# Optimization experiments

Hardware: AMD Instinct MI355X
Metric: run time of the kernel (lower is better)

## Reference

```python
import jax, jax.numpy as jnp
import numpy as np

EMB_DIM = 1024
ATT_DIM = 1024

def setup_inputs() -> dict:
    key = jax.random.key(0)
    ks = jax.random.split(key, 7)
    B, S = 8, 2048
    x_h = jax.random.normal(ks[0], (B, S, EMB_DIM), dtype=jnp.float32)
    # Linear params (stored as [in, out] for x @ W + b)
    sq = 1.0 / np.sqrt(EMB_DIM)
    Wq = jax.random.uniform(ks[1], (EMB_DIM, ATT_DIM), jnp.float32, -sq, sq)
    bq = jax.random.uniform(ks[2], (ATT_DIM,), jnp.float32, -sq, sq)
    Wk = jax.random.uniform(ks[3], (EMB_DIM, ATT_DIM), jnp.float32, -sq, sq)
    bk = jax.random.uniform(ks[4], (ATT_DIM,), jnp.float32, -sq, sq)
    Wv = jax.random.uniform(ks[5], (EMB_DIM, EMB_DIM), jnp.float32, -sq, sq)
    bv = jax.random.uniform(ks[6], (EMB_DIM,), jnp.float32, -sq, sq)
    return {"x_h": x_h, "Wq": Wq, "bq": bq, "Wk": Wk, "bk": bk, "Wv": Wv, "bv": bv}

def reference(x_h, Wq, bq, Wk, bk, Wv, bv):
    q = x_h @ Wq + bq               # [B,S,att_dim]
    k = x_h @ Wk + bk               # [B,S,att_dim]
    v = x_h @ Wv + bv               # [B,S,emb_dim]
    scale = 1.0 / jnp.sqrt(jnp.asarray(k.shape[-1], q.dtype))
    scores = jnp.einsum('bqd,bkd->bqk', q, k) * scale   # [B,S,S]
    # NOTE: original softmaxes over dim=1 (the QUERY axis), not the key axis.
    attn = jax.nn.softmax(scores, axis=1)
    return jnp.einsum('bqk,bkd->bqd', attn, v)
```

## Files before the change

kernel.cpp:

```cpp
#include <hip/hip_runtime.h>
#include <math.h>

typedef __bf16 bf16x8 __attribute__((ext_vector_type(8)));
typedef float f32x4 __attribute__((ext_vector_type(4)));
typedef unsigned short ushort8 __attribute__((ext_vector_type(8)));
typedef unsigned short ushort4v __attribute__((ext_vector_type(4)));
typedef unsigned short u16;

#define DEVINL __device__ __forceinline__

DEVINL u16 f2bf(float f) {
    union { float f; unsigned u; } a; a.f = f;
    unsigned u = a.u;
    return (u16)((u + 0x7FFFu + ((u >> 16) & 1u)) >> 16);
}
DEVINL float bf2f(u16 h) { return __uint_as_float(((unsigned)h) << 16); }

DEVINL void gload_lds16(const void* g, void* l) {
    __builtin_amdgcn_global_load_lds(
        (__attribute__((address_space(1))) void*)(g),
        (__attribute__((address_space(3))) void*)(l),
        16, 0, 0);
}

template<int EPI>
__global__ __launch_bounds__(512, 2)
void gemm256(const u16* __restrict__ A, int lda, long sAz,
             const u16* __restrict__ B, int ldb, long sBz,
             void* __restrict__ Cv, int ldc, long sCz,
             const float* __restrict__ bias, float* __restrict__ part,
             float scale, int K)
{
    __shared__ u16 lds[65536];
    const int tid = threadIdx.x;
    const int tile_x = blockIdx.x, tile_y = blockIdx.y;
    const long bz = blockIdx.z;

    const u16* Ab = A + bz * sAz;
    const u16* Bb = B + bz * sBz;
    const int row0 = tile_x * 256, col0 = tile_y * 256;

    const int sr = tid >> 2;
    const int csw = ((tid & 3) * 16) ^ (((sr >> 1) & 3) << 4);
    const u16* Ag = Ab + (long)(row0 + sr) * lda + (csw >> 1);
    const u16* Bg = Bb + (long)(col0 + sr) * ldb + (csw >> 1);
    const int dst0 = tid * 8;

    const int lane = tid & 63, wid = tid >> 6;
    const int wm = wid >> 2, wn = wid & 3;
    const int lane_r = lane & 15;
    const int rdcol = (((lane >> 4) * 16) ^ (((lane_r >> 1) & 3) << 4)) >> 1;
    const int arow0 = wm * 128 + lane_r;
    const int brow0 = wn * 64 + lane_r;

    const int NP = K >> 5;
    f32x4 acc[8][4] = {};

    auto issuePair = [&](int j2) {
        const int r = (j2 & 3) * 8192;
        const u16* ga = Ag + (long)j2 * 32;
        const u16* gb = Bg + (long)j2 * 32;
        gload_lds16(ga,                      &lds[r + dst0]);
        gload_lds16(ga + (long)128 * lda,    &lds[r + 4096 + dst0]);
        gload_lds16(gb,                      &lds[32768 + r + dst0]);
        gload_lds16(gb + (long)128 * ldb,    &lds[32768 + r + 4096 + dst0]);
    };

#define PHASE_BODY(JV)                                                      \
    {                                                                       \
        const int r = ((JV) & 3) * 8192;                                    \
        bf16x8 bfr[4], af[8];                                               \
        _Pragma("unroll")                                                   \
        for (int n = 0; n < 4; ++n)                                         \
            bfr[n] = *(const bf16x8*)&lds[32768 + r +                       \
                         (brow0 + n * 16) * 32 + rdcol];                    \
        _Pragma("unroll")                                                   \
        for (int m = 0; m < 8; ++m)                                         \
            af[m] = *(const bf16x8*)&lds[r + (arow0 + m * 16) * 32 + rdcol];\
        __builtin_amdgcn_s_setprio(1);                                      \
        _Pragma("unroll")                                                   \
        for (int m = 0; m < 8; ++m)                                         \
            _Pragma("unroll")                                               \
            for (int n = 0; n < 4; ++n)                                     \
                acc[m][n] = __builtin_amdgcn_mfma_f32_16x16x32_bf16(        \
                    bfr[n], af[m], acc[m][n], 0, 0, 0);                     \
        __builtin_amdgcn_s_setprio(0);                                      \
    }

    issuePair(0); issuePair(1); issuePair(2);
    asm volatile("s_waitcnt vmcnt(8)" ::: "memory");
    __builtin_amdgcn_s_barrier();

    for (int j = 0; j < NP - 3; ++j) {
        issuePair(j + 3);
        PHASE_BODY(j);
        asm volatile("s_waitcnt vmcnt(8)" ::: "memory");
        __builtin_amdgcn_s_barrier();
    }
    PHASE_BODY(NP - 3);
    asm volatile("s_waitcnt vmcnt(4)" ::: "memory");
    __builtin_amdgcn_s_barrier();
    PHASE_BODY(NP - 2);
    asm volatile("s_waitcnt vmcnt(0)" ::: "memory");
    __builtin_amdgcn_s_barrier();
    PHASE_BODY(NP - 1);
#undef PHASE_BODY

    const int erow = lane & 15, ecol0 = (lane >> 4) * 4;
    float4 bias4[4];
    if constexpr (EPI == 0) {
#pragma unroll
        for (int nf = 0; nf < 4; ++nf)
            bias4[nf] = *(const float4*)&bias[col0 + wn * 64 + nf * 16 + ecol0];
    }
    f32x4 csum[4] = {};
#pragma unroll
    for (int mf = 0; mf < 8; ++mf) {
        const int gr = row0 + wm * 128 + mf * 16 + erow;
#pragma unroll
        for (int nf = 0; nf < 4; ++nf) {
            const int gc = col0 + wn * 64 + nf * 16 + ecol0;
            f32x4 v = acc[mf][nf];
            if constexpr (EPI == 0) {
                v[0] += bias4[nf].x; v[1] += bias4[nf].y;
                v[2] += bias4[nf].z; v[3] += bias4[nf].w;
                ushort4v o = { f2bf(v[0]), f2bf(v[1]), f2bf(v[2]), f2bf(v[3]) };
                *(ushort4v*)((u16*)Cv + bz * sCz + (long)gr * ldc + gc) = o;
            } else if constexpr (EPI == 1) {
                f32x4 e;
#pragma unroll
                for (int r = 0; r < 4; ++r) e[r] = __expf(v[r] * scale);
                csum[nf] += e;
                ushort4v o = { f2bf(e[0]), f2bf(e[1]), f2bf(e[2]), f2bf(e[3]) };
                *(ushort4v*)((u16*)Cv + bz * sCz + (long)gr * ldc + gc) = o;
            } else {
                *(float4*)((float*)Cv + bz * sCz + (long)gr * ldc + gc) =
                    make_float4(v[0], v[1], v[2], v[3]);
            }
        }
    }
    if constexpr (EPI == 1) {
#pragma unroll
        for (int nf = 0; nf < 4; ++nf)
#pragma unroll
            for (int r = 0; r < 4; ++r) {
                float s = csum[nf][r];
                s += __shfl_xor(s, 1);
                s += __shfl_xor(s, 2);
                s += __shfl_xor(s, 4);
                s += __shfl_xor(s, 8);
                csum[nf][r] = s;
            }
        if ((lane & 15) == 0) {
#pragma unroll
            for (int nf = 0; nf < 4; ++nf) {
                float* p = part + ((bz * 16 + (long)tile_x * 2 + wm) * 2048)
                         + col0 + wn * 64 + nf * 16 + ecol0;
                *(float4*)p = make_float4(csum[nf][0], csum[nf][1],
                                          csum[nf][2], csum[nf][3]);
            }
        }
    }
}

__global__ void cast_x_k(const float* __restrict__ x, u16* __restrict__ o)
{
    const int i = blockIdx.x * 256 + threadIdx.x;
    const float4* xv = (const float4*)x;
    const float4 a = xv[(long)i * 2], b = xv[(long)i * 2 + 1];
    ushort8 r;
    r[0] = f2bf(a.x); r[1] = f2bf(a.y); r[2] = f2bf(a.z); r[3] = f2bf(a.w);
    r[4] = f2bf(b.x); r[5] = f2bf(b.y); r[6] = f2bf(b.z); r[7] = f2bf(b.w);
    *(ushort8*)(o + (long)i * 8) = r;
}

__global__ void wt_k(const float* __restrict__ Wq, const float* __restrict__ Wk,
                     const float* __restrict__ Wv, u16* __restrict__ Wt)
{
    __shared__ float t[32][33];
    const int z = blockIdx.z;
    const float* W = (z == 0) ? Wq : ((z == 1) ? Wk : Wv);
    const int k0 = blockIdx.x * 32, n0 = blockIdx.y * 32;
    const int tx = threadIdx.x, ty = threadIdx.y;
#pragma unroll
    for (int j = 0; j < 32; j += 8)
        t[ty + j][tx] = W[(long)(k0 + ty + j) * 1024 + n0 + tx];
    __syncthreads();
#pragma unroll
    for (int j = 0; j < 32; j += 8)
        Wt[((long)z * 1024 + n0 + ty + j) * 1024 + k0 + tx] = f2bf(t[tx][ty + j]);
}

__global__ void bias_k(const float* __restrict__ bq, const float* __restrict__ bk,
                       const float* __restrict__ bv, float* __restrict__ bcat)
{
    const int i = blockIdx.x * 256 + threadIdx.x;
    bcat[i] = (i < 1024) ? bq[i] : ((i < 2048) ? bk[i - 1024] : bv[i - 2048]);
}

__global__ void rcp_k(const float* __restrict__ part, float* __restrict__ rden)
{
    const int b = blockIdx.y;
    const int k = blockIdx.x * 256 + threadIdx.x;
    float s = 0.f;
#pragma unroll
    for (int c = 0; c < 16; ++c) s += part[((long)b * 16 + c) * 2048 + k];
    rden[b * 2048 + k] = 1.0f / s;
}

__global__ void vt_k(const u16* __restrict__ qkv, const float* __restrict__ rden,
                     u16* __restrict__ Vt)
{
    __shared__ float t[32][33];
    const int b = blockIdx.z;
    const int k0 = blockIdx.x * 32, d0 = blockIdx.y * 32;
    const int tx = threadIdx.x, ty = threadIdx.y;
#pragma unroll
    for (int j = 0; j < 32; j += 8) {
        const int k = k0 + ty + j;
        t[ty + j][tx] = bf2f(qkv[((long)b * 2048 + k) * 3072 + 2048 + d0 + tx])
                        * rden[b * 2048 + k];
    }
    __syncthreads();
#pragma unroll
    for (int j = 0; j < 32; j += 8)
        Vt[((long)b * 1024 + d0 + ty + j) * 2048 + k0 + tx] = f2bf(t[tx][ty + j]);
}

extern "C" void kernel_launch(void* const* d_in, const int* in_sizes, int n_in,
                              void* d_out, int out_size, void* d_ws, size_t ws_size,
                              hipStream_t stream)
{
    const float* x  = (const float*)d_in[0];
    const float* Wq = (const float*)d_in[1];
    const float* bq = (const float*)d_in[2];
    const float* Wk = (const float*)d_in[3];
    const float* bk = (const float*)d_in[4];
    const float* Wv = (const float*)d_in[5];
    const float* bv = (const float*)d_in[6];

    char* ws = (char*)d_ws;
    u16*   qkv  = (u16*)(ws);
    u16*   E    = (u16*)(ws + 100663296);
    u16*   Vt   = (u16*)(ws + 167772160);
    u16*   xb   = (u16*)(ws + 201326592);
    u16*   Wt   = (u16*)(ws + 234881024);
    float* bcat = (float*)(ws + 241172480);
    float* part = (float*)(ws + 241184768);
    float* rden = (float*)(ws + 243281920);

    const long sQKV = (long)2048 * 3072;
    const long sE   = (long)2048 * 2048;
    const long sVt  = (long)1024 * 2048;
    const long sO   = (long)2048 * 1024;

    cast_x_k<<<8192, 256, 0, stream>>>(x, xb);
    wt_k<<<dim3(32, 32, 3), dim3(32, 8), 0, stream>>>(Wq, Wk, Wv, Wt);
    bias_k<<<12, 256, 0, stream>>>(bq, bk, bv, bcat);
    gemm256<0><<<dim3(64, 12, 1), 512, 0, stream>>>(
        xb, 1024, 0, Wt, 1024, 0, qkv, 3072, 0, bcat, nullptr, 0.f, 1024);
    gemm256<1><<<dim3(8, 8, 8), 512, 0, stream>>>(
        qkv, 3072, sQKV, qkv + 1024, 3072, sQKV, E, 2048, sE,
        nullptr, part, 0.03125f, 1024);
    rcp_k<<<dim3(8, 8), 256, 0, stream>>>(part, rden);
    vt_k<<<dim3(64, 32, 8), dim3(32, 8), 0, stream>>>(qkv, rden, Vt);
    gemm256<2><<<dim3(8, 4, 8), 512, 0, stream>>>(
        E, 2048, sE, Vt, 2048, sVt, d_out, 1024, sO,
        nullptr, nullptr, 1.f, 2048);
}
```

Measured before the change: 307.8 us.

## Shrink GEMM tiles to 256x128 with double-buffered LDS and higher occupancy

Replaces the 256x256 tile with a 4-stage LDS ring by a 256x128 tile with a 2-stage double buffer. Each of the 8 waves now computes a 64x64 sub-tile, and launch bounds allow 4 blocks per CU. Grids double, and the softmax partial-sum layout and its reduction grow from 16 to 32 chunks. The aim is more blocks for better CU fill and latency hiding, at the cost of lower arithmetic intensity per tile, a shallower prefetch pipeline, and a full vmcnt(0) wait every K step.

```diff
diff --git a/kernel.cpp b/kernel.cpp
--- a/kernel.cpp
+++ b/kernel.cpp
@@ -24,21 +24,21 @@
 }
 
 template<int EPI>
-__global__ __launch_bounds__(512, 2)
-void gemm256(const u16* __restrict__ A, int lda, long sAz,
-             const u16* __restrict__ B, int ldb, long sBz,
-             void* __restrict__ Cv, int ldc, long sCz,
-             const float* __restrict__ bias, float* __restrict__ part,
-             float scale, int K)
-{
-    __shared__ u16 lds[65536];
+__global__ __launch_bounds__(512, 4)
+void gemm_t(const u16* __restrict__ A, int lda, long sAz,
+            const u16* __restrict__ B, int ldb, long sBz,
+            void* __restrict__ Cv, int ldc, long sCz,
+            const float* __restrict__ bias, float* __restrict__ part,
+            float scale, int K)
+{
+    __shared__ u16 lds[24576];
     const int tid = threadIdx.x;
     const int tile_x = blockIdx.x, tile_y = blockIdx.y;
     const long bz = blockIdx.z;
 
     const u16* Ab = A + bz * sAz;
     const u16* Bb = B + bz * sBz;
-    const int row0 = tile_x * 256, col0 = tile_y * 256;
+    const int row0 = tile_x * 256, col0 = tile_y * 128;
 
     const int sr = tid >> 2;
     const int csw = ((tid & 3) * 16) ^ (((sr >> 1) & 3) << 4);
@@ -47,64 +47,49 @@
     const int dst0 = tid * 8;
 
     const int lane = tid & 63, wid = tid >> 6;
-    const int wm = wid >> 2, wn = wid & 3;
+    const int wm = wid >> 1, wn = wid & 1;
     const int lane_r = lane & 15;
     const int rdcol = (((lane >> 4) * 16) ^ (((lane_r >> 1) & 3) << 4)) >> 1;
-    const int arow0 = wm * 128 + lane_r;
+    const int arow0 = wm * 64 + lane_r;
     const int brow0 = wn * 64 + lane_r;
 
-    const int NP = K >> 5;
-    f32x4 acc[8][4] = {};
-
-    auto issuePair = [&](int j2) {
-        const int r = (j2 & 3) * 8192;
-        const u16* ga = Ag + (long)j2 * 32;
-        const u16* gb = Bg + (long)j2 * 32;
-        gload_lds16(ga,                      &lds[r + dst0]);
-        gload_lds16(ga + (long)128 * lda,    &lds[r + 4096 + dst0]);
-        gload_lds16(gb,                      &lds[32768 + r + dst0]);
-        gload_lds16(gb + (long)128 * ldb,    &lds[32768 + r + 4096 + dst0]);
+    const int NT = K >> 5;
+    f32x4 acc[4][4] = {};
+
+    auto issuePair = [&](int j) {
+        const int base = (j & 1) * 12288;
+        const u16* ga = Ag + (long)j * 32;
+        gload_lds16(ga,                   &lds[base + dst0]);
+        gload_lds16(ga + (long)128 * lda, &lds[base + 4096 + dst0]);
+        gload_lds16(Bg + (long)j * 32,    &lds[base + 8192 + dst0]);
     };
 
-#define PHASE_BODY(JV)                                                      \
-    {                                                                       \
-        const int r = ((JV) & 3) * 8192;                                    \
-        bf16x8 bfr[4], af[8];                                               \
-        _Pragma("unroll")                                                   \
-        for (int n = 0; n < 4; ++n)                                         \
-            bfr[n] = *(const bf16x8*)&lds[32768 + r +                       \
-                         (brow0 + n * 16) * 32 + rdcol];                    \
-        _Pragma("unroll")                                                   \
-        for (int m = 0; m < 8; ++m)                                         \
-            af[m] = *(const bf16x8*)&lds[r + (arow0 + m * 16) * 32 + rdcol];\
-        __builtin_amdgcn_s_setprio(1);                                      \
-        _Pragma("unroll")                                                   \
-        for (int m = 0; m < 8; ++m)                                         \
-            _Pragma("unroll")                                               \
-            for (int n = 0; n < 4; ++n)                                     \
-                acc[m][n] = __builtin_amdgcn_mfma_f32_16x16x32_bf16(        \
-                    bfr[n], af[m], acc[m][n], 0, 0, 0);                     \
-        __builtin_amdgcn_s_setprio(0);                                      \
-    }
-
-    issuePair(0); issuePair(1); issuePair(2);
-    asm volatile("s_waitcnt vmcnt(8)" ::: "memory");
-    __builtin_amdgcn_s_barrier();
-
-    for (int j = 0; j < NP - 3; ++j) {
-        issuePair(j + 3);
-        PHASE_BODY(j);
-        asm volatile("s_waitcnt vmcnt(8)" ::: "memory");
-        __builtin_amdgcn_s_barrier();
-    }
-    PHASE_BODY(NP - 3);
-    asm volatile("s_waitcnt vmcnt(4)" ::: "memory");
-    __builtin_amdgcn_s_barrier();
-    PHASE_BODY(NP - 2);
+    issuePair(0);
     asm volatile("s_waitcnt vmcnt(0)" ::: "memory");
     __builtin_amdgcn_s_barrier();
-    PHASE_BODY(NP - 1);
-#undef PHASE_BODY
+
+    for (int j = 0; j < NT; ++j) {
+        if (j < NT - 1) issuePair(j + 1);
+        const int base = (j & 1) * 12288;
+        bf16x8 af[4], bfr[4];
+#pragma unroll
+        for (int n = 0; n < 4; ++n)
+            bfr[n] = *(const bf16x8*)&lds[base + 8192 +
+                         (brow0 + n * 16) * 32 + rdcol];
+#pragma unroll
+        for (int m = 0; m < 4; ++m)
+            af[m] = *(const bf16x8*)&lds[base + (arow0 + m * 16) * 32 + rdcol];
+        __builtin_amdgcn_s_setprio(1);
+#pragma unroll
+        for (int m = 0; m < 4; ++m)
+#pragma unroll
+            for (int n = 0; n < 4; ++n)
+                acc[m][n] = __builtin_amdgcn_mfma_f32_16x16x32_bf16(
+                    bfr[n], af[m], acc[m][n], 0, 0, 0);
+        __builtin_amdgcn_s_setprio(0);
+        asm volatile("s_waitcnt vmcnt(0)" ::: "memory");
+        __builtin_amdgcn_s_barrier();
+    }
 
     const int erow = lane & 15, ecol0 = (lane >> 4) * 4;
     float4 bias4[4];
@@ -115,8 +100,8 @@
     }
     f32x4 csum[4] = {};
 #pragma unroll
-    for (int mf = 0; mf < 8; ++mf) {
-        const int gr = row0 + wm * 128 + mf * 16 + erow;
+    for (int mf = 0; mf < 4; ++mf) {
+        const int gr = row0 + wm * 64 + mf * 16 + erow;
 #pragma unroll
         for (int nf = 0; nf < 4; ++nf) {
             const int gc = col0 + wn * 64 + nf * 16 + ecol0;
@@ -154,7 +139,7 @@
         if ((lane & 15) == 0) {
 #pragma unroll
             for (int nf = 0; nf < 4; ++nf) {
-                float* p = part + ((bz * 16 + (long)tile_x * 2 + wm) * 2048)
+                float* p = part + ((bz * 32 + (long)tile_x * 4 + wm) * 2048)
                          + col0 + wn * 64 + nf * 16 + ecol0;
                 *(float4*)p = make_float4(csum[nf][0], csum[nf][1],
                                           csum[nf][2], csum[nf][3]);
@@ -204,7 +189,7 @@
     const int k = blockIdx.x * 256 + threadIdx.x;
     float s = 0.f;
 #pragma unroll
-    for (int c = 0; c < 16; ++c) s += part[((long)b * 16 + c) * 2048 + k];
+    for (int c = 0; c < 32; ++c) s += part[((long)b * 32 + c) * 2048 + k];
     rden[b * 2048 + k] = 1.0f / s;
 }
 
@@ -257,14 +242,14 @@
     cast_x_k<<<8192, 256, 0, stream>>>(x, xb);
     wt_k<<<dim3(32, 32, 3), dim3(32, 8), 0, stream>>>(Wq, Wk, Wv, Wt);
     bias_k<<<12, 256, 0, stream>>>(bq, bk, bv, bcat);
-    gemm256<0><<<dim3(64, 12, 1), 512, 0, stream>>>(
+    gemm_t<0><<<dim3(64, 24, 1), 512, 0, stream>>>(
         xb, 1024, 0, Wt, 1024, 0, qkv, 3072, 0, bcat, nullptr, 0.f, 1024);
-    gemm256<1><<<dim3(8, 8, 8), 512, 0, stream>>>(
+    gemm_t<1><<<dim3(8, 16, 8), 512, 0, stream>>>(
         qkv, 3072, sQKV, qkv + 1024, 3072, sQKV, E, 2048, sE,
         nullptr, part, 0.03125f, 1024);
     rcp_k<<<dim3(8, 8), 256, 0, stream>>>(part, rden);
     vt_k<<<dim3(64, 32, 8), dim3(32, 8), 0, stream>>>(qkv, rden, Vt);
-    gemm256<2><<<dim3(8, 4, 8), 512, 0, stream>>>(
+    gemm_t<2><<<dim3(8, 8, 8), 512, 0, stream>>>(
         E, 2048, sE, Vt, 2048, sVt, d_out, 1024, sO,
         nullptr, nullptr, 1.f, 2048);
 }
```

After: 331.2 us. +7.6%, slower.
